# Performance work log

Hardware: AMD Instinct MI355X
Metric: run time of the kernel (lower is better)

The kernel has to match this reference:

```python
import jax, jax.numpy as jnp
import numpy as np

DIMENSIONS = 10000
NUM_LEVELS = 500
NUM_CLASSES = 128
SIZE = 6
BATCH = 256
MAX_TEMPERATURE = 41.6
MIN_TEMPERATURE = -19.9


def setup_inputs() -> dict:
    key = jax.random.key(0)
    k_x, k_w, k_b, k_r, k_c = jax.random.split(key, 5)
    x = jax.random.normal(k_x, (BATCH, SIZE), dtype=jnp.float32)
    # Sinusoid projection params: weight [D, size] ~ N(0,1), bias [D] ~ U(0, 2*pi)
    W_proj = jax.random.normal(k_w, (DIMENSIONS, SIZE), dtype=jnp.float32)
    b_proj = jax.random.uniform(k_b, (DIMENSIONS,), dtype=jnp.float32) * (2.0 * np.pi)
    W_reg = jax.random.normal(k_r, (NUM_CLASSES, DIMENSIONS), dtype=jnp.float32)
    # Level codebook: bipolar +-1 hypervectors [500, D]
    codebook = jnp.where(jax.random.normal(k_c, (NUM_LEVELS, DIMENSIONS)) > 0, 1.0, -1.0).astype(jnp.float32)
    return {"x": x, "W_proj": W_proj, "b_proj": b_proj, "W_reg": W_reg, "codebook": codebook}


def reference(x, W_proj, b_proj, W_reg, codebook):
    # Sinusoid projection: cos(xW^T + b) * sin(xW^T)  -> [B, D]
    proj = x @ W_proj.T
    sample_hv = jnp.cos(proj + b_proj) * jnp.sin(proj)
    # hard_quantize: sign to {+1, -1}
    enc = jnp.where(sample_hv > 0, 1.0, -1.0).astype(x.dtype)
    # bind(W_reg, enc) -> [B, C, D]; dot_similarity with codebook -> [B, C, K].
    # Fused as a single trilinear contraction (avoids the B*C*D intermediate).
    sim = jnp.einsum('bd,cd,kd->bck', enc, W_reg, codebook)
    index = jnp.argmax(sim, axis=-1)  # [B, C]
    slope = MAX_TEMPERATURE - MIN_TEMPERATURE
    pred = index.astype(jnp.float32) / (NUM_LEVELS - 1) * slope + MIN_TEMPERATURE
    return pred
```

## Files before the change

kernel.cpp:

```cpp
#include <hip/hip_runtime.h>
#include <math.h>

#define B_SZ 256
#define S_SZ 6
#define D_SZ 10000
#define DP   10112
#define C_SZ 128
#define K_SZ 500
#define KP   512
#define NIT  (DP / 64)
#define THR  1.0f
#define RCAP 32768

typedef _Float16       half8 __attribute__((ext_vector_type(8)));
typedef float          f32x4 __attribute__((ext_vector_type(4)));
typedef float          f32x16 __attribute__((ext_vector_type(16)));
typedef unsigned int   u32x4v __attribute__((ext_vector_type(4)));
typedef unsigned short u16x4 __attribute__((ext_vector_type(4)));
typedef unsigned short u16x8 __attribute__((ext_vector_type(8)));
typedef unsigned int   u32x4b __attribute__((ext_vector_type(4)));

__device__ __forceinline__ void stage16(const void* g, void* l) {
    __builtin_amdgcn_global_load_lds(
        (const __attribute__((address_space(1))) unsigned int*)g,
        (__attribute__((address_space(3))) unsigned int*)l, 16, 0, 0);
}

__global__ void prep_fused(const float* __restrict__ cb, _Float16* __restrict__ cbp,
                           const float* __restrict__ wreg, _Float16* __restrict__ whi,
                           const float* __restrict__ x, const float* __restrict__ wp,
                           const float* __restrict__ bp, unsigned short* __restrict__ em,
                           int* __restrict__ counter) {
    if (blockIdx.x == 0 && blockIdx.y == 0 && threadIdx.x == 0) *counter = 0;
    const int d = blockIdx.x * 2048 + threadIdx.x * 8;
    if (d >= DP) return;
    const int y = blockIdx.y;
    if (y < KP) {
        const int k = y;
        half8 hv;
        if (k < K_SZ && d + 8 <= D_SZ) {
            const f32x4 v0 = *(const f32x4*)(cb + (size_t)k * D_SZ + d);
            const f32x4 v1 = *(const f32x4*)(cb + (size_t)k * D_SZ + d + 4);
            #pragma unroll
            for (int j = 0; j < 4; ++j) { hv[j] = (_Float16)v0[j]; hv[4 + j] = (_Float16)v1[j]; }
        } else {
            #pragma unroll
            for (int j = 0; j < 8; ++j)
                hv[j] = (_Float16)((k < K_SZ && d + j < D_SZ) ? cb[(size_t)k * D_SZ + d + j] : 0.0f);
        }
        *(half8*)(cbp + (size_t)k * DP + d) = hv;
    } else if (y < KP + C_SZ) {
        const int c = y - KP;
        half8 hv;
        if (d + 8 <= D_SZ) {
            const f32x4 v0 = *(const f32x4*)(wreg + (size_t)c * D_SZ + d);
            const f32x4 v1 = *(const f32x4*)(wreg + (size_t)c * D_SZ + d + 4);
            #pragma unroll
            for (int j = 0; j < 4; ++j) { hv[j] = (_Float16)v0[j]; hv[4 + j] = (_Float16)v1[j]; }
        } else {
            #pragma unroll
            for (int j = 0; j < 8; ++j)
                hv[j] = (_Float16)((d + j < D_SZ) ? wreg[(size_t)c * D_SZ + d + j] : 0.0f);
        }
        *(half8*)(whi + (size_t)c * DP + d) = hv;
    } else {
        const int b = y - KP - C_SZ;
        u16x8 mv;
        if (d + 8 <= D_SZ) {
            float xv[S_SZ];
            #pragma unroll
            for (int s = 0; s < S_SZ; ++s) xv[s] = x[b * S_SZ + s];
            float wv[48];
            const float* wpd = wp + (size_t)d * S_SZ;
            #pragma unroll
            for (int q = 0; q < 12; ++q)
                *(f32x4*)(wv + q * 4) = *(const f32x4*)(wpd + q * 4);
            #pragma unroll
            for (int j = 0; j < 8; ++j) {
                double p = 0.0;
                #pragma unroll
                for (int s = 0; s < S_SZ; ++s)
                    p += (double)xv[s] * (double)wv[j * S_SZ + s];
                const double inv2pi = 0.15915494309189535;
                double t1 = p * inv2pi;
                double f1 = t1 - floor(t1);
                double t2 = (p + (double)bp[d + j]) * inv2pi;
                double f2 = t2 - floor(t2);
                bool sin_pos = (f1 < 0.5);
                bool cos_pos = (f2 < 0.25) || (f2 > 0.75);
                mv[j] = (sin_pos == cos_pos) ? (unsigned short)0u : (unsigned short)0x8000u;
            }
        } else {
            #pragma unroll
            for (int j = 0; j < 8; ++j) mv[j] = 0;
        }
        *(u16x8*)(em + (size_t)b * DP + d) = mv;
    }
}

__global__ __launch_bounds__(256, 2) void gemm_sim(
    const _Float16* __restrict__ whi, const _Float16* __restrict__ cbp,
    const unsigned short* __restrict__ em, _Float16* __restrict__ simh)
{
    const int kt = blockIdx.x >> 1;
    const int ct = blockIdx.x & 1;
    const int bg = blockIdx.y;
    const int tid  = threadIdx.x;
    const int wave = tid >> 6;
    const int lane = tid & 63;
    const int hi   = lane >> 5;
    const int l31  = lane & 31;
    const int swz  = lane & 7;

    __shared__ __align__(16) _Float16 s_whi[2][64 * 64];
    __shared__ __align__(16) _Float16 s_cb [2][64 * 64];
    __shared__ __align__(16) unsigned short s_mask[2][8 * 64];

    f32x16 acc[2][2][2];
    #pragma unroll
    for (int b = 0; b < 2; ++b)
        #pragma unroll
        for (int m = 0; m < 2; ++m)
            #pragma unroll
            for (int n = 0; n < 2; ++n)
                #pragma unroll
                for (int r = 0; r < 16; ++r)
                    acc[b][m][n][r] = 0.f;

    const int c0  = ct * 64;
    const int kr0 = kt * 64;
    const int bg8 = bg * 8;

    size_t abase[2], bbase[2];
    int soff[2];
    #pragma unroll
    for (int s = 0; s < 2; ++s) {
        int e = s * 256 + tid;
        int row = e >> 3;
        int p = e & 7;
        int gcol = (p ^ (row & 7)) * 8;
        abase[s] = (size_t)(c0 + row) * DP + gcol;
        bbase[s] = (size_t)(kr0 + row) * DP + gcol;
        soff[s] = e * 8;
    }
    const size_t embase = (size_t)(bg8 + (tid >> 3)) * DP + (tid & 7) * 8;

    auto STAGE = [&](int buf, int kb) {
        const int k0 = kb * 64;
        #pragma unroll
        for (int s = 0; s < 2; ++s) {
            stage16(whi + abase[s] + k0, &s_whi[buf][soff[s]]);
            stage16(cbp + bbase[s] + k0, &s_cb [buf][soff[s]]);
        }
        if (tid < 64)
            stage16(em + embase + k0, &s_mask[buf][tid * 8]);
    };

    STAGE(0, 0);
    __syncthreads();
    int cur = 0;

    for (int kb = 0; kb < NIT; ++kb) {
        if (kb + 1 < NIT) STAGE(cur ^ 1, kb + 1);

        const _Float16* ba = &s_whi[cur][0];
        const _Float16* bb = &s_cb [cur][0];
        const unsigned short* bm = &s_mask[cur][wave * 2 * 64];

        u32x4v ah[2][2], br[2][2], mr[2][2];
        {
            const int ch0 = (hi ^ swz) * 8;
            #pragma unroll
            for (int m = 0; m < 2; ++m)
                ah[0][m] = *(const u32x4v*)(ba + (m * 32 + l31) * 64 + ch0);
            #pragma unroll
            for (int n = 0; n < 2; ++n)
                br[0][n] = *(const u32x4v*)(bb + (n * 32 + l31) * 64 + ch0);
            #pragma unroll
            for (int b = 0; b < 2; ++b)
                mr[0][b] = *(const u32x4v*)(bm + b * 64 + hi * 8);
        }
        #pragma unroll
        for (int ks = 0; ks < 4; ++ks) {
            const int st = ks & 1;
            if (ks < 3) {
                const int nst = st ^ 1;
                const int ch = (((ks + 1) * 2 + hi) ^ swz) * 8;
                #pragma unroll
                for (int m = 0; m < 2; ++m)
                    ah[nst][m] = *(const u32x4v*)(ba + (m * 32 + l31) * 64 + ch);
                #pragma unroll
                for (int n = 0; n < 2; ++n)
                    br[nst][n] = *(const u32x4v*)(bb + (n * 32 + l31) * 64 + ch);
                #pragma unroll
                for (int b = 0; b < 2; ++b)
                    mr[nst][b] = *(const u32x4v*)(bm + b * 64 + (ks + 1) * 16 + hi * 8);
            }
            #pragma unroll
            for (int b = 0; b < 2; ++b) {
                half8 bs[2];
                #pragma unroll
                for (int n = 0; n < 2; ++n)
                    bs[n] = __builtin_bit_cast(half8, br[st][n] ^ mr[st][b]);
                #pragma unroll
                for (int m = 0; m < 2; ++m) {
                    half8 a = __builtin_bit_cast(half8, ah[st][m]);
                    #pragma unroll
                    for (int n = 0; n < 2; ++n)
                        acc[b][m][n] = __builtin_amdgcn_mfma_f32_32x32x16_f16(
                            a, bs[n], acc[b][m][n], 0, 0, 0);
                }
            }
        }
        __syncthreads();
        cur ^= 1;
    }

    #pragma unroll
    for (int b = 0; b < 2; ++b) {
        const size_t base = ((size_t)(bg8 + wave * 2 + b) * C_SZ + (size_t)c0) * KP;
        #pragma unroll
        for (int m = 0; m < 2; ++m)
            #pragma unroll
            for (int n = 0; n < 2; ++n) {
                const int kg = kr0 + n * 32 + l31;
                #pragma unroll
                for (int r = 0; r < 16; ++r) {
                    const int cl = m * 32 + (r & 3) + 8 * (r >> 2) + 4 * hi;
                    simh[base + (size_t)cl * KP + kg] = (_Float16)acc[b][m][n][r];
                }
            }
    }
}

__global__ __launch_bounds__(256) void argmax_gap(
    const _Float16* __restrict__ simh, float* __restrict__ out,
    int* __restrict__ counter, int* __restrict__ list)
{
    const int wave = threadIdx.x >> 6, lane = threadIdx.x & 63;
    const int row = blockIdx.x * 4 + wave;
    const half8 v = *(const half8*)(simh + (size_t)row * KP + lane * 8);
    float bv = -3.0e38f, bv2 = -3.0e38f; int bk = 0x7fffffff;
    #pragma unroll
    for (int j = 0; j < 8; ++j) {
        const int k = lane * 8 + j;
        const float f = (k < K_SZ) ? (float)v[j] : -3.0e38f;
        if (f > bv)       { bv2 = bv; bv = f; bk = k; }
        else if (f > bv2) { bv2 = f; }
    }
    #pragma unroll
    for (int off = 1; off < 64; off <<= 1) {
        const float ov  = __shfl_xor(bv,  off, 64);
        const int   ok  = __shfl_xor(bk,  off, 64);
        const float ov2 = __shfl_xor(bv2, off, 64);
        if (ov > bv || (ov == bv && ok < bk)) { bv2 = fmaxf(bv, ov2); bv = ov; bk = ok; }
        else                                  { bv2 = fmaxf(ov, bv2); }
    }
    if (lane == 0) {
        out[row] = (float)bk * (61.5f / 499.0f) - 19.9f;
        if (bv - bv2 < THR) {
            const int idx = atomicAdd(counter, 1);
            if (idx < RCAP) list[idx] = row;
        }
    }
}

__global__ __launch_bounds__(256) void repair(
    const _Float16* __restrict__ simh, const int* __restrict__ list,
    const int* __restrict__ counter, const unsigned short* __restrict__ em,
    const float* __restrict__ wreg, const _Float16* __restrict__ cbp,
    float* __restrict__ out)
{
    const int wave = threadIdx.x >> 6, lane = threadIdx.x & 63;
    const int wid = blockIdx.x * 4 + wave;
    const int nw  = gridDim.x * 4;
    int n = *counter;
    if (n > RCAP) n = RCAP;
    for (int i = wid; i < n; i += nw) {
        const int row = list[i];
        const int b = row >> 7, c = row & 127;
        const half8 v = *(const half8*)(simh + (size_t)row * KP + lane * 8);
        float vf[8];
        float mx = -3.0e38f;
        #pragma unroll
        for (int j = 0; j < 8; ++j) {
            const int k = lane * 8 + j;
            vf[j] = (k < K_SZ) ? (float)v[j] : -3.0e38f;
            mx = fmaxf(mx, vf[j]);
        }
        #pragma unroll
        for (int off = 1; off < 64; off <<= 1)
            mx = fmaxf(mx, __shfl_xor(mx, off, 64));
        const float thr = mx - THR;

        const float* wr = wreg + (size_t)c * D_SZ;
        const unsigned short* eb = em + (size_t)b * DP;

        double best = -1.0e300; int bestk = 0x7fffffff;
        #pragma unroll
        for (int j = 0; j < 8; ++j) {
            unsigned long long bal = __ballot(vf[j] >= thr);
            while (bal) {
                const int l = __ffsll((long long)bal) - 1;
                bal &= bal - 1;
                const int k = l * 8 + j;
                const unsigned short* ck = (const unsigned short*)(cbp + (size_t)k * DP);
                double s0 = 0.0, s1 = 0.0, s2 = 0.0, s3 = 0.0;
                for (int d = lane * 4; d < D_SZ; d += 256) {
                    const f32x4 w  = *(const f32x4*)(wr + d);
                    const u16x4 e4 = *(const u16x4*)(eb + d);
                    const u16x4 c4 = *(const u16x4*)(ck + d);
                    const u32x4b wb = __builtin_bit_cast(u32x4b, w);
                    u32x4b sb;
                    #pragma unroll
                    for (int q = 0; q < 4; ++q)
                        sb[q] = wb[q] ^ ((unsigned int)((e4[q] ^ c4[q]) & 0x8000u) << 16);
                    const f32x4 ws = __builtin_bit_cast(f32x4, sb);
                    s0 += (double)ws[0];
                    s1 += (double)ws[1];
                    s2 += (double)ws[2];
                    s3 += (double)ws[3];
                }
                double s = (s0 + s1) + (s2 + s3);
                #pragma unroll
                for (int off = 1; off < 64; off <<= 1)
                    s += __shfl_xor(s, off, 64);
                if (s > best || (s == best && k < bestk)) { best = s; bestk = k; }
            }
        }
        if (lane == 0)
            out[row] = (float)bestk * (61.5f / 499.0f) - 19.9f;
    }
}

extern "C" void kernel_launch(void* const* d_in, const int* in_sizes, int n_in,
                              void* d_out, int out_size, void* d_ws, size_t ws_size,
                              hipStream_t stream) {
    const float* x    = (const float*)d_in[0];
    const float* wp   = (const float*)d_in[1];
    const float* bp   = (const float*)d_in[2];
    const float* wreg = (const float*)d_in[3];
    const float* cb   = (const float*)d_in[4];
    float* out = (float*)d_out;

    char* ws = (char*)d_ws;
    size_t o = 0;
    auto take = [&](size_t bytes) -> char* {
        o = (o + 255) & ~(size_t)255;
        char* p = ws + o;
        o += bytes;
        return p;
    };
    _Float16* whi       = (_Float16*)take(sizeof(_Float16) * C_SZ * DP);
    _Float16* cbp       = (_Float16*)take(sizeof(_Float16) * KP * DP);
    unsigned short* em  = (unsigned short*)take(sizeof(unsigned short) * B_SZ * DP);
    _Float16* simh      = (_Float16*)take(sizeof(_Float16) * (size_t)B_SZ * C_SZ * KP);
    int* counter        = (int*)take(sizeof(int));
    int* list           = (int*)take(sizeof(int) * RCAP);
    (void)ws_size; (void)in_sizes; (void)n_in; (void)out_size;

    dim3 gp(5, KP + C_SZ + B_SZ);
    prep_fused<<<gp, 256, 0, stream>>>(cb, cbp, wreg, whi, x, wp, bp, em, counter);

    dim3 g(16, 32);
    gemm_sim<<<g, 256, 0, stream>>>(whi, cbp, em, simh);

    argmax_gap<<<(B_SZ * C_SZ) / 4, 256, 0, stream>>>(simh, out, counter, list);
    repair<<<1024, 256, 0, stream>>>(simh, list, counter, em, wreg, cbp, out);
}
```

Before: 393.1 us.

## Switch GEMM to 16x16x32 MFMA with 128-wide K tiles per stage

Replaces the 32x32x16 MFMA tiling with 16x16x32 MFMA tiles (4x4 per wave per batch pair) and doubles the K-chunk staged into LDS per iteration from 64 to 128, halving the number of loop iterations and barriers. The LDS swizzle is adapted to the 128-column rows. LDS usage doubles, which may reduce occupancy, and the 16x16 instruction issues more MFMAs for the same work.

Result: faster. 374.0 us (-4.9%).

```diff
diff --git a/kernel.cpp b/kernel.cpp
--- a/kernel.cpp
+++ b/kernel.cpp
@@ -8,13 +8,12 @@
 #define C_SZ 128
 #define K_SZ 500
 #define KP   512
-#define NIT  (DP / 64)
+#define NIT2 (DP / 128)
 #define THR  1.0f
 #define RCAP 32768
 
 typedef _Float16       half8 __attribute__((ext_vector_type(8)));
 typedef float          f32x4 __attribute__((ext_vector_type(4)));
-typedef float          f32x16 __attribute__((ext_vector_type(16)));
 typedef unsigned int   u32x4v __attribute__((ext_vector_type(4)));
 typedef unsigned short u16x4 __attribute__((ext_vector_type(4)));
 typedef unsigned short u16x8 __attribute__((ext_vector_type(8)));
@@ -108,51 +107,49 @@
     const int tid  = threadIdx.x;
     const int wave = tid >> 6;
     const int lane = tid & 63;
-    const int hi   = lane >> 5;
-    const int l31  = lane & 31;
-    const int swz  = lane & 7;
-
-    __shared__ __align__(16) _Float16 s_whi[2][64 * 64];
-    __shared__ __align__(16) _Float16 s_cb [2][64 * 64];
-    __shared__ __align__(16) unsigned short s_mask[2][8 * 64];
-
-    f32x16 acc[2][2][2];
+    const int quad = lane >> 4;
+    const int col  = lane & 15;
+
+    __shared__ __align__(16) _Float16 s_whi[2][64 * 128];
+    __shared__ __align__(16) _Float16 s_cb [2][64 * 128];
+    __shared__ __align__(16) unsigned short s_mask[2][8 * 128];
+
+    f32x4 acc[2][4][4];
     #pragma unroll
     for (int b = 0; b < 2; ++b)
         #pragma unroll
-        for (int m = 0; m < 2; ++m)
-            #pragma unroll
-            for (int n = 0; n < 2; ++n)
-                #pragma unroll
-                for (int r = 0; r < 16; ++r)
-                    acc[b][m][n][r] = 0.f;
+        for (int m = 0; m < 4; ++m)
+            #pragma unroll
+            for (int n = 0; n < 4; ++n)
+                acc[b][m][n] = (f32x4){0.f, 0.f, 0.f, 0.f};
 
     const int c0  = ct * 64;
     const int kr0 = kt * 64;
     const int bg8 = bg * 8;
 
-    size_t abase[2], bbase[2];
-    int soff[2];
-    #pragma unroll
-    for (int s = 0; s < 2; ++s) {
+    size_t abase[4], bbase[4];
+    int soff[4];
+    #pragma unroll
+    for (int s = 0; s < 4; ++s) {
         int e = s * 256 + tid;
-        int row = e >> 3;
-        int p = e & 7;
-        int gcol = (p ^ (row & 7)) * 8;
+        int row = e >> 4;
+        int p = e & 15;
+        int g = (p & 8) | ((p & 7) ^ (row & 7));
+        int gcol = g * 8;
         abase[s] = (size_t)(c0 + row) * DP + gcol;
         bbase[s] = (size_t)(kr0 + row) * DP + gcol;
         soff[s] = e * 8;
     }
-    const size_t embase = (size_t)(bg8 + (tid >> 3)) * DP + (tid & 7) * 8;
+    const size_t embase = (size_t)(bg8 + (tid >> 4)) * DP + (tid & 15) * 8;
 
     auto STAGE = [&](int buf, int kb) {
-        const int k0 = kb * 64;
-        #pragma unroll
-        for (int s = 0; s < 2; ++s) {
+        const int k0 = kb * 128;
+        #pragma unroll
+        for (int s = 0; s < 4; ++s) {
             stage16(whi + abase[s] + k0, &s_whi[buf][soff[s]]);
             stage16(cbp + bbase[s] + k0, &s_cb [buf][soff[s]]);
         }
-        if (tid < 64)
+        if (tid < 128)
             stage16(em + embase + k0, &s_mask[buf][tid * 8]);
     };
 
@@ -160,54 +157,55 @@
     __syncthreads();
     int cur = 0;
 
-    for (int kb = 0; kb < NIT; ++kb) {
-        if (kb + 1 < NIT) STAGE(cur ^ 1, kb + 1);
+    for (int kb = 0; kb < NIT2; ++kb) {
+        if (kb + 1 < NIT2) STAGE(cur ^ 1, kb + 1);
 
         const _Float16* ba = &s_whi[cur][0];
         const _Float16* bb = &s_cb [cur][0];
-        const unsigned short* bm = &s_mask[cur][wave * 2 * 64];
-
-        u32x4v ah[2][2], br[2][2], mr[2][2];
+        const unsigned short* bm = &s_mask[cur][wave * 2 * 128];
+
+        u32x4v ah[2][4], br[2][4], mr[2][2];
         {
-            const int ch0 = (hi ^ swz) * 8;
-            #pragma unroll
-            for (int m = 0; m < 2; ++m)
-                ah[0][m] = *(const u32x4v*)(ba + (m * 32 + l31) * 64 + ch0);
-            #pragma unroll
-            for (int n = 0; n < 2; ++n)
-                br[0][n] = *(const u32x4v*)(bb + (n * 32 + l31) * 64 + ch0);
+            const int off = ((quad ^ (col & 7)) * 8);
+            #pragma unroll
+            for (int m = 0; m < 4; ++m)
+                ah[0][m] = *(const u32x4v*)(ba + (m * 16 + col) * 128 + off);
+            #pragma unroll
+            for (int n = 0; n < 4; ++n)
+                br[0][n] = *(const u32x4v*)(bb + (n * 16 + col) * 128 + off);
             #pragma unroll
             for (int b = 0; b < 2; ++b)
-                mr[0][b] = *(const u32x4v*)(bm + b * 64 + hi * 8);
-        }
-        #pragma unroll
-        for (int ks = 0; ks < 4; ++ks) {
-            const int st = ks & 1;
-            if (ks < 3) {
+                mr[0][b] = *(const u32x4v*)(bm + b * 128 + quad * 8);
+        }
+        #pragma unroll
+        for (int k2 = 0; k2 < 4; ++k2) {
+            const int st = k2 & 1;
+            if (k2 < 3) {
                 const int nst = st ^ 1;
-                const int ch = (((ks + 1) * 2 + hi) ^ swz) * 8;
-                #pragma unroll
-                for (int m = 0; m < 2; ++m)
-                    ah[nst][m] = *(const u32x4v*)(ba + (m * 32 + l31) * 64 + ch);
-                #pragma unroll
-                for (int n = 0; n < 2; ++n)
-                    br[nst][n] = *(const u32x4v*)(bb + (n * 32 + l31) * 64 + ch);
+                const int C = (k2 + 1) * 4 + quad;
+                const int off = (C & 8) * 8 + ((C & 7) ^ (col & 7)) * 8;
+                #pragma unroll
+                for (int m = 0; m < 4; ++m)
+                    ah[nst][m] = *(const u32x4v*)(ba + (m * 16 + col) * 128 + off);
+                #pragma unroll
+                for (int n = 0; n < 4; ++n)
+                    br[nst][n] = *(const u32x4v*)(bb + (n * 16 + col) * 128 + off);
                 #pragma unroll
                 for (int b = 0; b < 2; ++b)
-                    mr[nst][b] = *(const u32x4v*)(bm + b * 64 + (ks + 1) * 16 + hi * 8);
+                    mr[nst][b] = *(const u32x4v*)(bm + b * 128 + C * 8);
             }
             #pragma unroll
             for (int b = 0; b < 2; ++b) {
-                half8 bs[2];
-                #pragma unroll
-                for (int n = 0; n < 2; ++n)
+                half8 bs[4];
+                #pragma unroll
+                for (int n = 0; n < 4; ++n)
                     bs[n] = __builtin_bit_cast(half8, br[st][n] ^ mr[st][b]);
                 #pragma unroll
-                for (int m = 0; m < 2; ++m) {
+                for (int m = 0; m < 4; ++m) {
                     half8 a = __builtin_bit_cast(half8, ah[st][m]);
                     #pragma unroll
-                    for (int n = 0; n < 2; ++n)
-                        acc[b][m][n] = __builtin_amdgcn_mfma_f32_32x32x16_f16(
+                    for (int n = 0; n < 4; ++n)
+                        acc[b][m][n] = __builtin_amdgcn_mfma_f32_16x16x32_f16(
                             a, bs[n], acc[b][m][n], 0, 0, 0);
                 }
             }
@@ -220,13 +218,13 @@
     for (int b = 0; b < 2; ++b) {
         const size_t base = ((size_t)(bg8 + wave * 2 + b) * C_SZ + (size_t)c0) * KP;
         #pragma unroll
-        for (int m = 0; m < 2; ++m)
-            #pragma unroll
-            for (int n = 0; n < 2; ++n) {
-                const int kg = kr0 + n * 32 + l31;
-                #pragma unroll
-                for (int r = 0; r < 16; ++r) {
-                    const int cl = m * 32 + (r & 3) + 8 * (r >> 2) + 4 * hi;
+        for (int m = 0; m < 4; ++m)
+            #pragma unroll
+            for (int n = 0; n < 4; ++n) {
+                const int kg = kr0 + n * 16 + col;
+                #pragma unroll
+                for (int r = 0; r < 4; ++r) {
+                    const int cl = m * 16 + quad * 4 + r;
                     simh[base + (size_t)cl * KP + kg] = (_Float16)acc[b][m][n][r];
                 }
             }
```

## Store fp16 operands in chunk-major layout for contiguous GEMM staging

Applied to the files above, without the earlier changes.

Replaces the row-major fp16 copies of W_reg and the codebook with a chunk-major layout ([D/8][rows][8]) built by a new LDS-transposing prep kernel. Each K-block then stages from one contiguous region instead of 64 strided rows, and the swizzle and register double-buffering in the MFMA loop are dropped. The repair kernel now reads the original fp32 codebook instead of the fp16 copy. The trade-offs are an extra kernel launch, the transpose cost, and no register prefetch of LDS fragments.

New measurement: 388.5 us. Within noise of the previous version (-1.2%).

```diff
diff --git a/kernel.cpp b/kernel.cpp
--- a/kernel.cpp
+++ b/kernel.cpp
@@ -5,6 +5,7 @@
 #define S_SZ 6
 #define D_SZ 10000
 #define DP   10112
+#define NCH  (DP / 8)
 #define C_SZ 128
 #define K_SZ 500
 #define KP   512
@@ -26,80 +27,98 @@
         (__attribute__((address_space(3))) unsigned int*)l, 16, 0, 0);
 }
 
-__global__ void prep_fused(const float* __restrict__ cb, _Float16* __restrict__ cbp,
-                           const float* __restrict__ wreg, _Float16* __restrict__ whi,
-                           const float* __restrict__ x, const float* __restrict__ wp,
-                           const float* __restrict__ bp, unsigned short* __restrict__ em,
-                           int* __restrict__ counter) {
+__global__ void prep_transpose(const float* __restrict__ cb, _Float16* __restrict__ cbT,
+                               const float* __restrict__ wreg, _Float16* __restrict__ whiT) {
+    __shared__ _Float16 lt[64 * 64];
+    const int t  = threadIdx.x;
+    const int dt = blockIdx.x;
+    const int y  = blockIdx.y;
+    const bool is_cb = (y < 8);
+    const int rt = is_cb ? y * 64 : (y - 8) * 64;
+    const int Rv = is_cb ? K_SZ : C_SZ;
+    const int Ro = is_cb ? KP : C_SZ;
+    const float* src = is_cb ? cb : wreg;
+    _Float16* dst = is_cb ? cbT : whiT;
+
+    {
+        const int r = t >> 2, q = t & 3;
+        const int gr = rt + r;
+        const int d0 = dt * 64 + q * 16;
+        _Float16 hv[16];
+        #pragma unroll
+        for (int j = 0; j < 4; ++j) {
+            const int d = d0 + j * 4;
+            if (gr < Rv && d + 4 <= D_SZ) {
+                const f32x4 v = *(const f32x4*)(src + (size_t)gr * D_SZ + d);
+                #pragma unroll
+                for (int e = 0; e < 4; ++e) hv[j * 4 + e] = (_Float16)v[e];
+            } else {
+                #pragma unroll
+                for (int e = 0; e < 4; ++e)
+                    hv[j * 4 + e] = (_Float16)((gr < Rv && d + e < D_SZ)
+                                               ? src[(size_t)gr * D_SZ + d + e] : 0.0f);
+            }
+        }
+        #pragma unroll
+        for (int h = 0; h < 2; ++h) {
+            const int g = q * 2 + h;
+            half8 v8;
+            #pragma unroll
+            for (int e = 0; e < 8; ++e) v8[e] = hv[h * 8 + e];
+            *(half8*)(lt + r * 64 + ((g ^ (r & 7)) * 8)) = v8;
+        }
+    }
+    __syncthreads();
+    #pragma unroll
+    for (int s = 0; s < 2; ++s) {
+        const int slot = s * 256 + t;
+        const int g = slot >> 6, r = slot & 63;
+        const half8 v8 = *(const half8*)(lt + r * 64 + ((g ^ (r & 7)) * 8));
+        *(half8*)(dst + ((size_t)(dt * 8 + g) * Ro + rt + r) * 8) = v8;
+    }
+}
+
+__global__ void prep_enc(const float* __restrict__ x, const float* __restrict__ wp,
+                         const float* __restrict__ bp, unsigned short* __restrict__ em,
+                         int* __restrict__ counter) {
     if (blockIdx.x == 0 && blockIdx.y == 0 && threadIdx.x == 0) *counter = 0;
     const int d = blockIdx.x * 2048 + threadIdx.x * 8;
     if (d >= DP) return;
-    const int y = blockIdx.y;
-    if (y < KP) {
-        const int k = y;
-        half8 hv;
-        if (k < K_SZ && d + 8 <= D_SZ) {
-            const f32x4 v0 = *(const f32x4*)(cb + (size_t)k * D_SZ + d);
-            const f32x4 v1 = *(const f32x4*)(cb + (size_t)k * D_SZ + d + 4);
-            #pragma unroll
-            for (int j = 0; j < 4; ++j) { hv[j] = (_Float16)v0[j]; hv[4 + j] = (_Float16)v1[j]; }
-        } else {
-            #pragma unroll
-            for (int j = 0; j < 8; ++j)
-                hv[j] = (_Float16)((k < K_SZ && d + j < D_SZ) ? cb[(size_t)k * D_SZ + d + j] : 0.0f);
-        }
-        *(half8*)(cbp + (size_t)k * DP + d) = hv;
-    } else if (y < KP + C_SZ) {
-        const int c = y - KP;
-        half8 hv;
-        if (d + 8 <= D_SZ) {
-            const f32x4 v0 = *(const f32x4*)(wreg + (size_t)c * D_SZ + d);
-            const f32x4 v1 = *(const f32x4*)(wreg + (size_t)c * D_SZ + d + 4);
-            #pragma unroll
-            for (int j = 0; j < 4; ++j) { hv[j] = (_Float16)v0[j]; hv[4 + j] = (_Float16)v1[j]; }
-        } else {
-            #pragma unroll
-            for (int j = 0; j < 8; ++j)
-                hv[j] = (_Float16)((d + j < D_SZ) ? wreg[(size_t)c * D_SZ + d + j] : 0.0f);
-        }
-        *(half8*)(whi + (size_t)c * DP + d) = hv;
+    const int b = blockIdx.y;
+    u16x8 mv;
+    if (d + 8 <= D_SZ) {
+        float xv[S_SZ];
+        #pragma unroll
+        for (int s = 0; s < S_SZ; ++s) xv[s] = x[b * S_SZ + s];
+        float wv[48];
+        const float* wpd = wp + (size_t)d * S_SZ;
+        #pragma unroll
+        for (int q = 0; q < 12; ++q)
+            *(f32x4*)(wv + q * 4) = *(const f32x4*)(wpd + q * 4);
+        #pragma unroll
+        for (int j = 0; j < 8; ++j) {
+            double p = 0.0;
+            #pragma unroll
+            for (int s = 0; s < S_SZ; ++s)
+                p += (double)xv[s] * (double)wv[j * S_SZ + s];
+            const double inv2pi = 0.15915494309189535;
+            double t1 = p * inv2pi;
+            double f1 = t1 - floor(t1);
+            double t2 = (p + (double)bp[d + j]) * inv2pi;
+            double f2 = t2 - floor(t2);
+            bool sin_pos = (f1 < 0.5);
+            bool cos_pos = (f2 < 0.25) || (f2 > 0.75);
+            mv[j] = (sin_pos == cos_pos) ? (unsigned short)0u : (unsigned short)0x8000u;
+        }
     } else {
-        const int b = y - KP - C_SZ;
-        u16x8 mv;
-        if (d + 8 <= D_SZ) {
-            float xv[S_SZ];
-            #pragma unroll
-            for (int s = 0; s < S_SZ; ++s) xv[s] = x[b * S_SZ + s];
-            float wv[48];
-            const float* wpd = wp + (size_t)d * S_SZ;
-            #pragma unroll
-            for (int q = 0; q < 12; ++q)
-                *(f32x4*)(wv + q * 4) = *(const f32x4*)(wpd + q * 4);
-            #pragma unroll
-            for (int j = 0; j < 8; ++j) {
-                double p = 0.0;
-                #pragma unroll
-                for (int s = 0; s < S_SZ; ++s)
-                    p += (double)xv[s] * (double)wv[j * S_SZ + s];
-                const double inv2pi = 0.15915494309189535;
-                double t1 = p * inv2pi;
-                double f1 = t1 - floor(t1);
-                double t2 = (p + (double)bp[d + j]) * inv2pi;
-                double f2 = t2 - floor(t2);
-                bool sin_pos = (f1 < 0.5);
-                bool cos_pos = (f2 < 0.25) || (f2 > 0.75);
-                mv[j] = (sin_pos == cos_pos) ? (unsigned short)0u : (unsigned short)0x8000u;
-            }
-        } else {
-            #pragma unroll
-            for (int j = 0; j < 8; ++j) mv[j] = 0;
-        }
-        *(u16x8*)(em + (size_t)b * DP + d) = mv;
-    }
+        #pragma unroll
+        for (int j = 0; j < 8; ++j) mv[j] = 0;
+    }
+    *(u16x8*)(em + (size_t)b * DP + d) = mv;
 }
 
 __global__ __launch_bounds__(256, 2) void gemm_sim(
-    const _Float16* __restrict__ whi, const _Float16* __restrict__ cbp,
+    const _Float16* __restrict__ whiT, const _Float16* __restrict__ cbT,
     const unsigned short* __restrict__ em, _Float16* __restrict__ simh)
 {
     const int kt = blockIdx.x >> 1;
@@ -110,10 +129,9 @@
     const int lane = tid & 63;
     const int hi   = lane >> 5;
     const int l31  = lane & 31;
-    const int swz  = lane & 7;
-
-    __shared__ __align__(16) _Float16 s_whi[2][64 * 64];
-    __shared__ __align__(16) _Float16 s_cb [2][64 * 64];
+
+    __shared__ __align__(16) _Float16 s_whi[2][8 * 64 * 8];
+    __shared__ __align__(16) _Float16 s_cb [2][8 * 64 * 8];
     __shared__ __align__(16) unsigned short s_mask[2][8 * 64];
 
     f32x16 acc[2][2][2];
@@ -131,80 +149,64 @@
     const int kr0 = kt * 64;
     const int bg8 = bg * 8;
 
-    size_t abase[2], bbase[2];
-    int soff[2];
+    int aoff[2], boff[2], soff[2];
     #pragma unroll
     for (int s = 0; s < 2; ++s) {
-        int e = s * 256 + tid;
-        int row = e >> 3;
-        int p = e & 7;
-        int gcol = (p ^ (row & 7)) * 8;
-        abase[s] = (size_t)(c0 + row) * DP + gcol;
-        bbase[s] = (size_t)(kr0 + row) * DP + gcol;
+        const int e = s * 256 + tid;
+        const int ch = e >> 6, row = e & 63;
+        aoff[s] = (ch * C_SZ + c0 + row) * 8;
+        boff[s] = (ch * KP  + kr0 + row) * 8;
         soff[s] = e * 8;
     }
     const size_t embase = (size_t)(bg8 + (tid >> 3)) * DP + (tid & 7) * 8;
 
     auto STAGE = [&](int buf, int kb) {
-        const int k0 = kb * 64;
+        const _Float16* baA = whiT + (size_t)kb * 8 * C_SZ * 8;
+        const _Float16* baB = cbT  + (size_t)kb * 8 * KP  * 8;
         #pragma unroll
         for (int s = 0; s < 2; ++s) {
-            stage16(whi + abase[s] + k0, &s_whi[buf][soff[s]]);
-            stage16(cbp + bbase[s] + k0, &s_cb [buf][soff[s]]);
+            stage16(baA + aoff[s], &s_whi[buf][soff[s]]);
+            stage16(baB + boff[s], &s_cb [buf][soff[s]]);
         }
         if (tid < 64)
-            stage16(em + embase + k0, &s_mask[buf][tid * 8]);
+            stage16(em + embase + kb * 64, &s_mask[buf][tid * 8]);
     };
 
     STAGE(0, 0);
     __syncthreads();
     int cur = 0;
 
+    const int fAB = (hi * 64 + l31) * 8;
+    const int fM  = (wave * 2) * 64 + hi * 8;
+
     for (int kb = 0; kb < NIT; ++kb) {
         if (kb + 1 < NIT) STAGE(cur ^ 1, kb + 1);
 
         const _Float16* ba = &s_whi[cur][0];
         const _Float16* bb = &s_cb [cur][0];
-        const unsigned short* bm = &s_mask[cur][wave * 2 * 64];
-
-        u32x4v ah[2][2], br[2][2], mr[2][2];
-        {
-            const int ch0 = (hi ^ swz) * 8;
+        const unsigned short* bm = &s_mask[cur][0];
+
+        #pragma unroll
+        for (int ks = 0; ks < 4; ++ks) {
+            u32x4v ah[2], br[2], mr[2];
             #pragma unroll
             for (int m = 0; m < 2; ++m)
-                ah[0][m] = *(const u32x4v*)(ba + (m * 32 + l31) * 64 + ch0);
+                ah[m] = *(const u32x4v*)(ba + fAB + ks * 1024 + m * 256);
             #pragma unroll
             for (int n = 0; n < 2; ++n)
-                br[0][n] = *(const u32x4v*)(bb + (n * 32 + l31) * 64 + ch0);
+                br[n] = *(const u32x4v*)(bb + fAB + ks * 1024 + n * 256);
             #pragma unroll
             for (int b = 0; b < 2; ++b)
-                mr[0][b] = *(const u32x4v*)(bm + b * 64 + hi * 8);
-        }
-        #pragma unroll
-        for (int ks = 0; ks < 4; ++ks) {
-            const int st = ks & 1;
-            if (ks < 3) {
-                const int nst = st ^ 1;
-                const int ch = (((ks + 1) * 2 + hi) ^ swz) * 8;
-                #pragma unroll
-                for (int m = 0; m < 2; ++m)
-                    ah[nst][m] = *(const u32x4v*)(ba + (m * 32 + l31) * 64 + ch);
-                #pragma unroll
-                for (int n = 0; n < 2; ++n)
-                    br[nst][n] = *(const u32x4v*)(bb + (n * 32 + l31) * 64 + ch);
-                #pragma unroll
-                for (int b = 0; b < 2; ++b)
-                    mr[nst][b] = *(const u32x4v*)(bm + b * 64 + (ks + 1) * 16 + hi * 8);
-            }
+                mr[b] = *(const u32x4v*)(bm + fM + b * 64 + ks * 16);
             #pragma unroll
             for (int b = 0; b < 2; ++b) {
                 half8 bs[2];
                 #pragma unroll
                 for (int n = 0; n < 2; ++n)
-                    bs[n] = __builtin_bit_cast(half8, br[st][n] ^ mr[st][b]);
+                    bs[n] = __builtin_bit_cast(half8, br[n] ^ mr[b]);
                 #pragma unroll
                 for (int m = 0; m < 2; ++m) {
-                    half8 a = __builtin_bit_cast(half8, ah[st][m]);
+                    half8 a = __builtin_bit_cast(half8, ah[m]);
                     #pragma unroll
                     for (int n = 0; n < 2; ++n)
                         acc[b][m][n] = __builtin_amdgcn_mfma_f32_32x32x16_f16(
@@ -268,7 +270,7 @@
 __global__ __launch_bounds__(256) void repair(
     const _Float16* __restrict__ simh, const int* __restrict__ list,
     const int* __restrict__ counter, const unsigned short* __restrict__ em,
-    const float* __restrict__ wreg, const _Float16* __restrict__ cbp,
+    const float* __restrict__ wreg, const float* __restrict__ cb,
     float* __restrict__ out)
 {
     const int wave = threadIdx.x >> 6, lane = threadIdx.x & 63;
@@ -304,17 +306,18 @@
                 const int l = __ffsll((long long)bal) - 1;
                 bal &= bal - 1;
                 const int k = l * 8 + j;
-                const unsigned short* ck = (const unsigned short*)(cbp + (size_t)k * DP);
+                const float* ck = cb + (size_t)k * D_SZ;
                 double s0 = 0.0, s1 = 0.0, s2 = 0.0, s3 = 0.0;
                 for (int d = lane * 4; d < D_SZ; d += 256) {
                     const f32x4 w  = *(const f32x4*)(wr + d);
                     const u16x4 e4 = *(const u16x4*)(eb + d);
-                    const u16x4 c4 = *(const u16x4*)(ck + d);
+                    const f32x4 cw = *(const f32x4*)(ck + d);
                     const u32x4b wb = __builtin_bit_cast(u32x4b, w);
+                    const u32x4b cbits = __builtin_bit_cast(u32x4b, cw);
                     u32x4b sb;
                     #pragma unroll
                     for (int q = 0; q < 4; ++q)
-                        sb[q] = wb[q] ^ ((unsigned int)((e4[q] ^ c4[q]) & 0x8000u) << 16);
+                        sb[q] = wb[q] ^ ((((unsigned int)e4[q] << 16) ^ cbits[q]) & 0x80000000u);
                     const f32x4 ws = __builtin_bit_cast(f32x4, sb);
                     s0 += (double)ws[0];
                     s1 += (double)ws[1];
@@ -351,20 +354,22 @@
         o += bytes;
         return p;
     };
-    _Float16* whi       = (_Float16*)take(sizeof(_Float16) * C_SZ * DP);
-    _Float16* cbp       = (_Float16*)take(sizeof(_Float16) * KP * DP);
+    _Float16* whiT      = (_Float16*)take(sizeof(_Float16) * (size_t)NCH * C_SZ * 8);
+    _Float16* cbT       = (_Float16*)take(sizeof(_Float16) * (size_t)NCH * KP * 8);
     unsigned short* em  = (unsigned short*)take(sizeof(unsigned short) * B_SZ * DP);
     _Float16* simh      = (_Float16*)take(sizeof(_Float16) * (size_t)B_SZ * C_SZ * KP);
     int* counter        = (int*)take(sizeof(int));
     int* list           = (int*)take(sizeof(int) * RCAP);
     (void)ws_size; (void)in_sizes; (void)n_in; (void)out_size;
 
-    dim3 gp(5, KP + C_SZ + B_SZ);
-    prep_fused<<<gp, 256, 0, stream>>>(cb, cbp, wreg, whi, x, wp, bp, em, counter);
+    dim3 gt(NIT, 10);
+    prep_transpose<<<gt, 256, 0, stream>>>(cb, cbT, wreg, whiT);
+    dim3 ge(5, B_SZ);
+    prep_enc<<<ge, 256, 0, stream>>>(x, wp, bp, em, counter);
 
     dim3 g(16, 32);
-    gemm_sim<<<g, 256, 0, stream>>>(whi, cbp, em, simh);
+    gemm_sim<<<g, 256, 0, stream>>>(whiT, cbT, em, simh);
 
     argmax_gap<<<(B_SZ * C_SZ) / 4, 256, 0, stream>>>(simh, out, counter, list);
-    repair<<<1024, 256, 0, stream>>>(simh, list, counter, em, wreg, cbp, out);
-}
+    repair<<<1024, 256, 0, stream>>>(simh, list, counter, em, wreg, cb, out);
+}
```
